# Kernel tuning notes

Measured on AMD Instinct MI355X. Metric: run time of the kernel, lower is better.

Reference implementation:

```python
import jax, jax.numpy as jnp
import numpy as np

B, T, D, H = 4, 2048, 1024, 16
HD = D // H
EPS = 1e-5


def gelu_tanh(x):
    c = jnp.sqrt(jnp.asarray(2.0 / jnp.pi, x.dtype))
    return 0.5 * x * (1.0 + jnp.tanh(c * (x + 0.044715 * x * x * x)))


def layernorm(x, gamma, beta):
    mean = jnp.mean(x, axis=-1, keepdims=True)
    var = jnp.var(x, axis=-1, keepdims=True)
    return gamma * (x - mean) / jnp.sqrt(var + EPS) + beta


def setup_inputs() -> dict:
    key = jax.random.key(0)
    ks = jax.random.split(key, 12)
    s = 0.02
    return {
        "x": jax.random.normal(ks[0], (B, T, D), jnp.float32),
        "Wq": jax.random.normal(ks[1], (D, D), jnp.float32) * s,
        "Wk": jax.random.normal(ks[2], (D, D), jnp.float32) * s,
        "Wv": jax.random.normal(ks[3], (D, D), jnp.float32) * s,
        "Wo": jax.random.normal(ks[4], (D, D), jnp.float32) * s,
        "bo": jnp.zeros((D,), jnp.float32),
        "W1": jax.random.normal(ks[5], (D, 4 * D), jnp.float32) * s,
        "b1": jnp.zeros((4 * D,), jnp.float32),
        "W2": jax.random.normal(ks[6], (4 * D, D), jnp.float32) * s,
        "b2": jnp.zeros((D,), jnp.float32),
        "gamma1": jnp.ones((D,), jnp.float32),
        "beta1": jnp.zeros((D,), jnp.float32),
        "gamma2": jnp.ones((D,), jnp.float32),
        "beta2": jnp.zeros((D,), jnp.float32),
    }


def reference(x, Wq, Wk, Wv, Wo, bo, W1, b1, W2, b2, gamma1, beta1, gamma2, beta2):
    # --- attention sublayer (pre-norm, causal) ---
    h = layernorm(x, gamma1, beta1)
    q = (h @ Wq).reshape(B, T, H, HD).transpose(0, 2, 1, 3)  # (B,H,T,hd)
    k = (h @ Wk).reshape(B, T, H, HD).transpose(0, 2, 1, 3)
    v = (h @ Wv).reshape(B, T, H, HD).transpose(0, 2, 1, 3)
    scores = jnp.einsum("bhqd,bhkd->bhqk", q, k) * (HD ** -0.5)
    causal = jnp.tril(jnp.ones((T, T), bool))
    scores = jnp.where(causal, scores, -jnp.inf)
    w = jax.nn.softmax(scores, axis=-1)
    attn = jnp.einsum("bhqk,bhkd->bhqd", w, v).transpose(0, 2, 1, 3).reshape(B, T, D)
    x = x + (attn @ Wo + bo)
    # --- FFN sublayer ---
    h2 = layernorm(x, gamma2, beta2)
    ff = gelu_tanh(h2 @ W1 + b1) @ W2 + b2
    return x + ff
```

## Files before the change

kernel.cpp:

```cpp
#include <hip/hip_runtime.h>
#include <hip/hip_bf16.h>


typedef __bf16 bf16;
typedef __attribute__((ext_vector_type(8))) __bf16 bf16x8;
typedef __attribute__((ext_vector_type(4))) __bf16 bf16x4;
typedef __attribute__((ext_vector_type(2))) __bf16 bf16x2;
typedef __attribute__((ext_vector_type(4))) float floatx4;

#define EXPC 0.18033688011112042f

__device__ __forceinline__ void async_cp16(const bf16* g, bf16* l) {
  __builtin_amdgcn_global_load_lds(
      (const __attribute__((address_space(1))) void*)g,
      (__attribute__((address_space(3))) void*)l, 16, 0, 0);
}

__global__ __launch_bounds__(256) void transpose_cvt4(
    const float* __restrict__ S0, const float* __restrict__ S1,
    const float* __restrict__ S2, const float* __restrict__ S3,
    bf16* __restrict__ D0, bf16* __restrict__ D1, bf16* __restrict__ D2,
    bf16* __restrict__ D3, int K, int N) {
  const float* W = (blockIdx.z == 0) ? S0 : (blockIdx.z == 1) ? S1
                   : (blockIdx.z == 2) ? S2 : S3;
  bf16* WT = (blockIdx.z == 0) ? D0 : (blockIdx.z == 1) ? D1
             : (blockIdx.z == 2) ? D2 : D3;
  __shared__ bf16 tile[32][33];
  const int tn = blockIdx.x;
  const int tk = blockIdx.y;
  const int t = threadIdx.x;
  const int row = t >> 3;
  const int c4 = (t & 7) * 4;

  const float* src = W + (size_t)(tk * 32 + row) * N + tn * 32 + c4;
  float4 v = *(const float4*)src;
  tile[row][c4 + 0] = (bf16)v.x;
  tile[row][c4 + 1] = (bf16)v.y;
  tile[row][c4 + 2] = (bf16)v.z;
  tile[row][c4 + 3] = (bf16)v.w;
  __syncthreads();
  bf16x4 o;
  o[0] = tile[c4 + 0][row];
  o[1] = tile[c4 + 1][row];
  o[2] = tile[c4 + 2][row];
  o[3] = tile[c4 + 3][row];
  *(bf16x4*)(WT + (size_t)(tn * 32 + row) * K + tk * 32 + c4) = o;
}

__global__ __launch_bounds__(256) void transpose_cvt(
    const float* __restrict__ W, bf16* __restrict__ WT, int K, int N) {
  __shared__ bf16 tile[32][33];
  const int tn = blockIdx.x;
  const int tk = blockIdx.y;
  const int t = threadIdx.x;
  const int row = t >> 3;
  const int c4 = (t & 7) * 4;

  const float* src = W + (size_t)(tk * 32 + row) * N + tn * 32 + c4;
  float4 v = *(const float4*)src;
  tile[row][c4 + 0] = (bf16)v.x;
  tile[row][c4 + 1] = (bf16)v.y;
  tile[row][c4 + 2] = (bf16)v.z;
  tile[row][c4 + 3] = (bf16)v.w;
  __syncthreads();
  bf16x4 o;
  o[0] = tile[c4 + 0][row];
  o[1] = tile[c4 + 1][row];
  o[2] = tile[c4 + 2][row];
  o[3] = tile[c4 + 3][row];
  *(bf16x4*)(WT + (size_t)(tn * 32 + row) * K + tk * 32 + c4) = o;
}

__global__ __launch_bounds__(256) void ln_kernel(
    const float* __restrict__ x, const float* __restrict__ gamma,
    const float* __restrict__ beta, bf16* __restrict__ out) {
  const int row = blockIdx.x;
  const int t = threadIdx.x;
  const float* xr = x + (size_t)row * 1024;
  float4 v4 = *(const float4*)(xr + t * 4);
  float a[4] = {v4.x, v4.y, v4.z, v4.w};
  float s = a[0] + a[1] + a[2] + a[3];
  float ss = a[0] * a[0] + a[1] * a[1] + a[2] * a[2] + a[3] * a[3];
  for (int off = 1; off < 64; off <<= 1) {
    s += __shfl_xor(s, off);
    ss += __shfl_xor(ss, off);
  }
  __shared__ float red[8];
  const int wid = t >> 6, lane = t & 63;
  if (lane == 0) { red[wid] = s; red[wid + 4] = ss; }
  __syncthreads();
  s = red[0] + red[1] + red[2] + red[3];
  ss = red[4] + red[5] + red[6] + red[7];
  const float mean = s * (1.0f / 1024.0f);
  const float var = ss * (1.0f / 1024.0f) - mean * mean;
  const float rstd = rsqrtf(var + 1e-5f);
  bf16x4 o;
  for (int j = 0; j < 4; ++j) {
    float g = gamma[t * 4 + j];
    float b = beta[t * 4 + j];
    o[j] = (bf16)((a[j] - mean) * rstd * g + b);
  }
  *(bf16x4*)(out + (size_t)row * 1024 + t * 4) = o;
}

__device__ __forceinline__ float gelu_f(float x) {
  const float c = 0.7978845608028654f;
  float u = c * (x + 0.044715f * x * x * x);
  u = fminf(fmaxf(u, -10.0f), 10.0f);
  float t = __builtin_exp2f(u * 2.8853900817779268f);
  return x * t * __builtin_amdgcn_rcpf(t + 1.0f);
}

template <int MODE, int BK>
__global__ __launch_bounds__(256, 2) void gemm_bt(
    const bf16* __restrict__ A, const bf16* __restrict__ BT,
    const float* __restrict__ bias, const float* __restrict__ resid,
    void* __restrict__ out, int M, int N, int K) {
  __shared__ bf16 sA[128 * BK];
  __shared__ bf16 sB[128 * BK];
  constexpr int GPR = BK / 8;
  constexpr int CPT = GPR / 2;
  constexpr int RPI = 256 / GPR;
  constexpr int SW = (BK >= 64) ? 7 : 0;

  const int t = threadIdx.x;
  const int lane = t & 63, wid = t >> 6;
  const int waveM = wid >> 1, waveN = wid & 1;
  const int quad = lane >> 4, l16 = lane & 15;
  const size_t m0 = (size_t)blockIdx.x * 128;
  const size_t n0 = (size_t)blockIdx.y * 128;

  floatx4 acc[4][4] = {};

  const int r0 = t / GPR;
  const int gp = t % GPR;
  const int gsrc = gp ^ (r0 & SW);
  const bf16* Ag = A + (m0 + r0) * (size_t)K + gsrc * 8;
  const bf16* Bg = BT + (n0 + r0) * (size_t)K + gsrc * 8;
  bf16* sAp = sA + t * 8;
  bf16* sBp = sB + t * 8;

  for (int k0 = 0; k0 < K; k0 += BK) {
    __syncthreads();
#pragma unroll
    for (int it = 0; it < CPT; ++it) {
      async_cp16(Ag + k0 + (size_t)(it * RPI) * K, sAp + it * 2048);
      async_cp16(Bg + k0 + (size_t)(it * RPI) * K, sBp + it * 2048);
    }
    __syncthreads();
#pragma unroll
    for (int ks = 0; ks < BK / 32; ++ks) {
      bf16x8 af[4], bfv[4];
#pragma unroll
      for (int i = 0; i < 4; ++i) {
        const int rowA = waveM * 64 + i * 16 + l16;
        const int g = ((ks * 4 + quad) ^ (l16 & SW)) * 8;
        af[i] = *(const bf16x8*)&sA[rowA * BK + g];
        const int rowB = waveN * 64 + i * 16 + l16;
        bfv[i] = *(const bf16x8*)&sB[rowB * BK + g];
      }
#pragma unroll
      for (int mt = 0; mt < 4; ++mt)
#pragma unroll
        for (int nt = 0; nt < 4; ++nt)
          acc[mt][nt] = __builtin_amdgcn_mfma_f32_16x16x32_bf16(
              af[mt], bfv[nt], acc[mt][nt], 0, 0, 0);
    }
  }

#pragma unroll
  for (int mt = 0; mt < 4; ++mt) {
#pragma unroll
    for (int nt = 0; nt < 4; ++nt) {
      const size_t row_base = m0 + waveM * 64 + mt * 16 + quad * 4;
      const size_t col = n0 + waveN * 64 + nt * 16 + l16;
#pragma unroll
      for (int r = 0; r < 4; ++r) {
        const size_t row = row_base + r;
        float v = acc[mt][nt][r];
        if (MODE == 1) {
          v = gelu_f(v + bias[col]);
          ((bf16*)out)[row * N + col] = (bf16)v;
        } else if (MODE == 2) {
          v += bias[col] + resid[row * N + col];
          ((float*)out)[row * N + col] = v;
        } else {
          ((bf16*)out)[row * N + col] = (bf16)v;
        }
      }
    }
  }
}

__global__ __launch_bounds__(256) void attn_kernel(
    const bf16* __restrict__ QKV, bf16* __restrict__ O) {
  const int idx = blockIdx.x;
  const int qt = 15 - (idx >> 6);
  const int bh = idx & 63;
  const int b = bh >> 4, h = bh & 15;
  const int t = threadIdx.x;
  const int lane = t & 63, wid = t >> 6;
  const int quad = lane >> 4, l16 = lane & 15;

  __shared__ bf16 sQ[128][72];
  __shared__ bf16 sK[64][72];
  __shared__ bf16 sVt[64][72];
  __shared__ bf16 sP[4][16][72];

  const size_t qbase = (size_t)b * 2048 * 3072 + (size_t)h * 64;
  const int q0 = qt * 128;

  for (int c = t; c < 1024; c += 256) {
    int row = c >> 3, sub = (c & 7) * 8;
    *(bf16x8*)&sQ[row][sub] =
        *(const bf16x8*)(QKV + qbase + (size_t)(q0 + row) * 3072 + sub);
  }
  __syncthreads();

  bf16x8 aq[2][2];
#pragma unroll
  for (int mt = 0; mt < 2; ++mt)
#pragma unroll
    for (int ks = 0; ks < 2; ++ks)
      aq[mt][ks] =
          *(const bf16x8*)&sQ[wid * 32 + mt * 16 + l16][ks * 32 + quad * 8];

  float l_part[2][4] = {};
  floatx4 o_acc[2][4] = {};

  const int kr = t >> 3;
  const int sub = (t & 7) * 8;
  const bf16* pK0 = QKV + qbase + 1024 + (size_t)kr * 3072 + sub;
  const bf16* pK1 = pK0 + (size_t)32 * 3072;
  const int vr = kr * 2;
  const bf16* pV0 = QKV + qbase + 2048 + (size_t)vr * 3072 + sub;
  const bf16* pV1 = pV0 + 3072;
  const int vcol = vr ^ (sub & 56);
  const ptrdiff_t bump = (ptrdiff_t)64 * 3072;

  const int ktmax = 2 * qt + 1;
  for (int kt = 0; kt <= ktmax; ++kt) {
    __syncthreads();
    *(bf16x8*)&sK[kr][sub] = *(const bf16x8*)pK0;
    *(bf16x8*)&sK[32 + kr][sub] = *(const bf16x8*)pK1;
    bf16x8 va = *(const bf16x8*)pV0;
    bf16x8 vb = *(const bf16x8*)pV1;
#pragma unroll
    for (int j = 0; j < 8; ++j) {
      bf16x2 pk = {va[j], vb[j]};
      *(bf16x2*)&sVt[sub + j][vcol] = pk;
    }
    pK0 += bump; pK1 += bump; pV0 += bump; pV1 += bump;
    __syncthreads();

    bf16x8 bv[4][2];
#pragma unroll
    for (int nt = 0; nt < 4; ++nt) {
      const int r2 = nt * 16 + l16;
#pragma unroll
      for (int ks = 0; ks < 2; ++ks)
        bv[nt][ks] =
            *(const bf16x8*)&sVt[r2][(ks * 32 + quad * 8) ^ (r2 & 56)];
    }

    float p[2][4][4];
#pragma unroll
    for (int nt = 0; nt < 4; ++nt) {
      const int r2 = nt * 16 + l16;
      bf16x8 bk0 = *(const bf16x8*)&sK[r2][quad * 8];
      bf16x8 bk1 = *(const bf16x8*)&sK[r2][32 + quad * 8];
#pragma unroll
      for (int mt = 0; mt < 2; ++mt) {
        floatx4 acc = {};
        acc = __builtin_amdgcn_mfma_f32_16x16x32_bf16(aq[mt][0], bk0, acc, 0, 0, 0);
        acc = __builtin_amdgcn_mfma_f32_16x16x32_bf16(aq[mt][1], bk1, acc, 0, 0, 0);
#pragma unroll
        for (int r = 0; r < 4; ++r)
          p[mt][nt][r] = __builtin_exp2f(acc[r] * EXPC);
      }
    }

    if (kt >= ktmax - 1) {
      const int k0 = kt * 64;
#pragma unroll
      for (int mt = 0; mt < 2; ++mt) {
        const int qrow_base = q0 + wid * 32 + mt * 16 + quad * 4;
#pragma unroll
        for (int nt = 0; nt < 4; ++nt) {
          const int kk = k0 + nt * 16 + l16;
#pragma unroll
          for (int r = 0; r < 4; ++r)
            if (kk > qrow_base + r) p[mt][nt][r] = 0.f;
        }
      }
    }

#pragma unroll
    for (int mt = 0; mt < 2; ++mt) {
#pragma unroll
      for (int nt = 0; nt < 4; ++nt)
#pragma unroll
        for (int r = 0; r < 4; ++r) {
          l_part[mt][r] += p[mt][nt][r];
          sP[wid][quad * 4 + r][nt * 16 + l16] = (bf16)p[mt][nt][r];
        }
      bf16x8 ap0 = *(const bf16x8*)&sP[wid][l16][quad * 8];
      bf16x8 ap1 = *(const bf16x8*)&sP[wid][l16][32 + quad * 8];
#pragma unroll
      for (int nt = 0; nt < 4; ++nt) {
        o_acc[mt][nt] = __builtin_amdgcn_mfma_f32_16x16x32_bf16(
            ap0, bv[nt][0], o_acc[mt][nt], 0, 0, 0);
        o_acc[mt][nt] = __builtin_amdgcn_mfma_f32_16x16x32_bf16(
            ap1, bv[nt][1], o_acc[mt][nt], 0, 0, 0);
      }
    }
  }

#pragma unroll
  for (int mt = 0; mt < 2; ++mt) {
#pragma unroll
    for (int off = 1; off < 16; off <<= 1)
#pragma unroll
      for (int r = 0; r < 4; ++r)
        l_part[mt][r] += __shfl_xor(l_part[mt][r], off);
    float inv[4];
#pragma unroll
    for (int r = 0; r < 4; ++r) inv[r] = 1.0f / l_part[mt][r];
#pragma unroll
    for (int nt = 0; nt < 4; ++nt)
#pragma unroll
      for (int r = 0; r < 4; ++r) {
        const size_t row =
            (size_t)b * 2048 + q0 + wid * 32 + mt * 16 + quad * 4 + r;
        const size_t col = (size_t)h * 64 + nt * 16 + l16;
        O[row * 1024 + col] = (bf16)(o_acc[mt][nt][r] * inv[r]);
      }
  }
}

extern "C" void kernel_launch(void* const* d_in, const int* in_sizes, int n_in,
                              void* d_out, int out_size, void* d_ws, size_t ws_size,
                              hipStream_t stream) {
  const float* x = (const float*)d_in[0];
  const float* Wq = (const float*)d_in[1];
  const float* Wk = (const float*)d_in[2];
  const float* Wv = (const float*)d_in[3];
  const float* Wo = (const float*)d_in[4];
  const float* bo = (const float*)d_in[5];
  const float* W1 = (const float*)d_in[6];
  const float* b1 = (const float*)d_in[7];
  const float* W2 = (const float*)d_in[8];
  const float* b2 = (const float*)d_in[9];
  const float* gamma1 = (const float*)d_in[10];
  const float* beta1 = (const float*)d_in[11];
  const float* gamma2 = (const float*)d_in[12];
  const float* beta2 = (const float*)d_in[13];

  char* ws = (char*)d_ws;
  const size_t MB = (size_t)1 << 20;
  bf16* WqkvT = (bf16*)(ws + 0 * MB);
  bf16* WoT = (bf16*)(ws + 6 * MB);
  bf16* W1T = (bf16*)(ws + 8 * MB);
  bf16* W2T = (bf16*)(ws + 16 * MB);
  bf16* h1  = (bf16*)(ws + 24 * MB);
  bf16* QKVb = (bf16*)(ws + 40 * MB);
  bf16* attnb = (bf16*)(ws + 88 * MB);
  float* x1 = (float*)(ws + 104 * MB);
  bf16* h2  = (bf16*)(ws + 136 * MB);
  bf16* midb = (bf16*)(ws + 152 * MB);

  dim3 blk(256);

  transpose_cvt4<<<dim3(32, 32, 4), blk, 0, stream>>>(
      Wq, Wk, Wv, Wo, WqkvT, WqkvT + (size_t)1024 * 1024,
      WqkvT + (size_t)2048 * 1024, WoT, 1024, 1024);
  transpose_cvt<<<dim3(128, 32), blk, 0, stream>>>(W1, W1T, 1024, 4096);
  transpose_cvt<<<dim3(32, 128), blk, 0, stream>>>(W2, W2T, 4096, 1024);

  ln_kernel<<<8192, blk, 0, stream>>>(x, gamma1, beta1, h1);

  gemm_bt<3, 64><<<dim3(64, 24), blk, 0, stream>>>(h1, WqkvT, nullptr, nullptr,
                                                   QKVb, 8192, 3072, 1024);

  attn_kernel<<<dim3(1024), blk, 0, stream>>>(QKVb, attnb);

  gemm_bt<2, 128><<<dim3(64, 8), blk, 0, stream>>>(attnb, WoT, bo, x, x1,
                                                   8192, 1024, 1024);

  ln_kernel<<<8192, blk, 0, stream>>>(x1, gamma2, beta2, h2);

  gemm_bt<1, 64><<<dim3(64, 32), blk, 0, stream>>>(h2, W1T, b1, nullptr, midb,
                                                   8192, 4096, 1024);

  gemm_bt<2, 128><<<dim3(64, 8), blk, 0, stream>>>(midb, W2T, b2, x1, d_out,
                                                   8192, 1024, 4096);
}
```

Measured before the change: 468.0 us.

## Pre-transpose V and use async global-to-LDS loads with XOR swizzle in attention

Adds a separate kernel that writes V transposed per head into workspace, which removes the in-loop scalar transpose-scatter into LDS. The attention kernel now loads Q, K and V^T straight into LDS with global_load_lds and an XOR-swizzled layout, and swaps the MFMA operands so P is stored as packed bf16x4 with a simpler row-sum reduction. The cost is an extra kernel launch and an extra pass over V through memory. Vt reuses h1's workspace region, which is already consumed by then.

```diff
diff --git a/kernel.cpp b/kernel.cpp
--- a/kernel.cpp
+++ b/kernel.cpp
@@ -5,7 +5,6 @@
 typedef __bf16 bf16;
 typedef __attribute__((ext_vector_type(8))) __bf16 bf16x8;
 typedef __attribute__((ext_vector_type(4))) __bf16 bf16x4;
-typedef __attribute__((ext_vector_type(2))) __bf16 bf16x2;
 typedef __attribute__((ext_vector_type(4))) float floatx4;
 
 #define EXPC 0.18033688011112042f
@@ -69,6 +68,31 @@
   o[2] = tile[c4 + 2][row];
   o[3] = tile[c4 + 3][row];
   *(bf16x4*)(WT + (size_t)(tn * 32 + row) * K + tk * 32 + c4) = o;
+}
+
+__global__ __launch_bounds__(256) void vtrans_kernel(
+    const bf16* __restrict__ QKV, bf16* __restrict__ Vt) {
+  const int tt = blockIdx.x;
+  const int bh = blockIdx.y;
+  const int b = bh >> 4, h = bh & 15;
+  __shared__ bf16 tile[64][72];
+  const int t = threadIdx.x;
+  const int row = t >> 3;
+  const int c8 = (t & 7) * 8;
+  const size_t vbase = (size_t)b * 2048 * 3072 + 2048 + (size_t)h * 64;
+  const bf16* src = QKV + vbase + (size_t)(tt * 64 + row) * 3072 + c8;
+  *(bf16x8*)&tile[row][c8] = *(const bf16x8*)src;
+  *(bf16x8*)&tile[row + 32][c8] = *(const bf16x8*)(src + (size_t)32 * 3072);
+  __syncthreads();
+  bf16x8 o0, o1;
+#pragma unroll
+  for (int j = 0; j < 8; ++j) {
+    o0[j] = tile[c8 + j][row];
+    o1[j] = tile[c8 + j][row + 32];
+  }
+  bf16* dst = Vt + ((size_t)bh * 64 + row) * 2048 + tt * 64 + c8;
+  *(bf16x8*)dst = o0;
+  *(bf16x8*)(dst + (size_t)32 * 2048) = o1;
 }
 
 __global__ __launch_bounds__(256) void ln_kernel(
@@ -193,7 +217,8 @@
 }
 
 __global__ __launch_bounds__(256) void attn_kernel(
-    const bf16* __restrict__ QKV, bf16* __restrict__ O) {
+    const bf16* __restrict__ QKV, const bf16* __restrict__ Vt,
+    bf16* __restrict__ O) {
   const int idx = blockIdx.x;
   const int qt = 15 - (idx >> 6);
   const int bh = idx & 63;
@@ -202,78 +227,76 @@
   const int lane = t & 63, wid = t >> 6;
   const int quad = lane >> 4, l16 = lane & 15;
 
-  __shared__ bf16 sQ[128][72];
-  __shared__ bf16 sK[64][72];
-  __shared__ bf16 sVt[64][72];
+  __shared__ bf16 sQ[128 * 64];
+  __shared__ bf16 sK[64 * 64];
+  __shared__ bf16 sV[64 * 64];
   __shared__ bf16 sP[4][16][72];
 
-  const size_t qbase = (size_t)b * 2048 * 3072 + (size_t)h * 64;
+  const size_t qkvbase = (size_t)b * 2048 * 3072 + (size_t)h * 64;
   const int q0 = qt * 128;
 
-  for (int c = t; c < 1024; c += 256) {
-    int row = c >> 3, sub = (c & 7) * 8;
-    *(bf16x8*)&sQ[row][sub] =
-        *(const bf16x8*)(QKV + qbase + (size_t)(q0 + row) * 3072 + sub);
-  }
+  const int r0 = t >> 3;
+  const int gp = t & 7;
+  const int gsw = gp ^ (r0 & 7);
+
+  {
+    const bf16* pQ = QKV + qkvbase + (size_t)(q0 + r0) * 3072 + gsw * 8;
+#pragma unroll
+    for (int j = 0; j < 4; ++j)
+      async_cp16(pQ + (size_t)(j * 32) * 3072, sQ + j * 2048 + t * 8);
+  }
+
+  const bf16* pK = QKV + qkvbase + 1024 + (size_t)r0 * 3072 + gsw * 8;
+  const bf16* pV = Vt + ((size_t)bh * 64 + r0) * 2048 + gsw * 8;
+  const ptrdiff_t bumpK = (ptrdiff_t)64 * 3072;
+
   __syncthreads();
 
   bf16x8 aq[2][2];
 #pragma unroll
-  for (int mt = 0; mt < 2; ++mt)
+  for (int mt = 0; mt < 2; ++mt) {
+    const int row = wid * 32 + mt * 16 + l16;
 #pragma unroll
     for (int ks = 0; ks < 2; ++ks)
       aq[mt][ks] =
-          *(const bf16x8*)&sQ[wid * 32 + mt * 16 + l16][ks * 32 + quad * 8];
-
-  float l_part[2][4] = {};
+          *(const bf16x8*)&sQ[row * 64 + (((ks * 4 + quad) ^ (row & 7)) * 8)];
+  }
+
+  float l_part[2] = {0.f, 0.f};
   floatx4 o_acc[2][4] = {};
-
-  const int kr = t >> 3;
-  const int sub = (t & 7) * 8;
-  const bf16* pK0 = QKV + qbase + 1024 + (size_t)kr * 3072 + sub;
-  const bf16* pK1 = pK0 + (size_t)32 * 3072;
-  const int vr = kr * 2;
-  const bf16* pV0 = QKV + qbase + 2048 + (size_t)vr * 3072 + sub;
-  const bf16* pV1 = pV0 + 3072;
-  const int vcol = vr ^ (sub & 56);
-  const ptrdiff_t bump = (ptrdiff_t)64 * 3072;
 
   const int ktmax = 2 * qt + 1;
   for (int kt = 0; kt <= ktmax; ++kt) {
     __syncthreads();
-    *(bf16x8*)&sK[kr][sub] = *(const bf16x8*)pK0;
-    *(bf16x8*)&sK[32 + kr][sub] = *(const bf16x8*)pK1;
-    bf16x8 va = *(const bf16x8*)pV0;
-    bf16x8 vb = *(const bf16x8*)pV1;
-#pragma unroll
-    for (int j = 0; j < 8; ++j) {
-      bf16x2 pk = {va[j], vb[j]};
-      *(bf16x2*)&sVt[sub + j][vcol] = pk;
-    }
-    pK0 += bump; pK1 += bump; pV0 += bump; pV1 += bump;
+    async_cp16(pK, sK + t * 8);
+    async_cp16(pK + (size_t)32 * 3072, sK + 2048 + t * 8);
+    async_cp16(pV, sV + t * 8);
+    async_cp16(pV + (size_t)32 * 2048, sV + 2048 + t * 8);
+    pK += bumpK;
+    pV += 64;
     __syncthreads();
 
     bf16x8 bv[4][2];
 #pragma unroll
     for (int nt = 0; nt < 4; ++nt) {
-      const int r2 = nt * 16 + l16;
+      const int d = nt * 16 + l16;
 #pragma unroll
       for (int ks = 0; ks < 2; ++ks)
         bv[nt][ks] =
-            *(const bf16x8*)&sVt[r2][(ks * 32 + quad * 8) ^ (r2 & 56)];
+            *(const bf16x8*)&sV[d * 64 + (((ks * 4 + quad) ^ (d & 7)) * 8)];
     }
 
     float p[2][4][4];
 #pragma unroll
     for (int nt = 0; nt < 4; ++nt) {
-      const int r2 = nt * 16 + l16;
-      bf16x8 bk0 = *(const bf16x8*)&sK[r2][quad * 8];
-      bf16x8 bk1 = *(const bf16x8*)&sK[r2][32 + quad * 8];
+      const int kr = nt * 16 + l16;
+      bf16x8 bk0 = *(const bf16x8*)&sK[kr * 64 + ((quad ^ (kr & 7)) * 8)];
+      bf16x8 bk1 = *(const bf16x8*)&sK[kr * 64 + (((4 + quad) ^ (kr & 7)) * 8)];
 #pragma unroll
       for (int mt = 0; mt < 2; ++mt) {
         floatx4 acc = {};
-        acc = __builtin_amdgcn_mfma_f32_16x16x32_bf16(aq[mt][0], bk0, acc, 0, 0, 0);
-        acc = __builtin_amdgcn_mfma_f32_16x16x32_bf16(aq[mt][1], bk1, acc, 0, 0, 0);
+        acc = __builtin_amdgcn_mfma_f32_16x16x32_bf16(bk0, aq[mt][0], acc, 0, 0, 0);
+        acc = __builtin_amdgcn_mfma_f32_16x16x32_bf16(bk1, aq[mt][1], acc, 0, 0, 0);
 #pragma unroll
         for (int r = 0; r < 4; ++r)
           p[mt][nt][r] = __builtin_exp2f(acc[r] * EXPC);
@@ -284,13 +307,13 @@
       const int k0 = kt * 64;
 #pragma unroll
       for (int mt = 0; mt < 2; ++mt) {
-        const int qrow_base = q0 + wid * 32 + mt * 16 + quad * 4;
+        const int qg = q0 + wid * 32 + mt * 16 + l16;
 #pragma unroll
         for (int nt = 0; nt < 4; ++nt) {
-          const int kk = k0 + nt * 16 + l16;
+          const int kg = k0 + nt * 16 + quad * 4;
 #pragma unroll
           for (int r = 0; r < 4; ++r)
-            if (kk > qrow_base + r) p[mt][nt][r] = 0.f;
+            if (kg + r > qg) p[mt][nt][r] = 0.f;
         }
       }
     }
@@ -298,12 +321,15 @@
 #pragma unroll
     for (int mt = 0; mt < 2; ++mt) {
 #pragma unroll
-      for (int nt = 0; nt < 4; ++nt)
+      for (int nt = 0; nt < 4; ++nt) {
+        bf16x4 pk;
 #pragma unroll
         for (int r = 0; r < 4; ++r) {
-          l_part[mt][r] += p[mt][nt][r];
-          sP[wid][quad * 4 + r][nt * 16 + l16] = (bf16)p[mt][nt][r];
+          l_part[mt] += p[mt][nt][r];
+          pk[r] = (bf16)p[mt][nt][r];
         }
+        *(bf16x4*)&sP[wid][l16][nt * 16 + quad * 4] = pk;
+      }
       bf16x8 ap0 = *(const bf16x8*)&sP[wid][l16][quad * 8];
       bf16x8 ap1 = *(const bf16x8*)&sP[wid][l16][32 + quad * 8];
 #pragma unroll
@@ -318,14 +344,13 @@
 
 #pragma unroll
   for (int mt = 0; mt < 2; ++mt) {
-#pragma unroll
-    for (int off = 1; off < 16; off <<= 1)
-#pragma unroll
-      for (int r = 0; r < 4; ++r)
-        l_part[mt][r] += __shfl_xor(l_part[mt][r], off);
+    float lt = l_part[mt];
+    lt += __shfl_xor(lt, 16);
+    lt += __shfl_xor(lt, 32);
     float inv[4];
 #pragma unroll
-    for (int r = 0; r < 4; ++r) inv[r] = 1.0f / l_part[mt][r];
+    for (int r = 0; r < 4; ++r)
+      inv[r] = 1.0f / __shfl(lt, quad * 4 + r);
 #pragma unroll
     for (int nt = 0; nt < 4; ++nt)
 #pragma unroll
@@ -363,6 +388,7 @@
   bf16* W1T = (bf16*)(ws + 8 * MB);
   bf16* W2T = (bf16*)(ws + 16 * MB);
   bf16* h1  = (bf16*)(ws + 24 * MB);
+  bf16* Vt  = (bf16*)(ws + 24 * MB);
   bf16* QKVb = (bf16*)(ws + 40 * MB);
   bf16* attnb = (bf16*)(ws + 88 * MB);
   float* x1 = (float*)(ws + 104 * MB);
@@ -382,7 +408,9 @@
   gemm_bt<3, 64><<<dim3(64, 24), blk, 0, stream>>>(h1, WqkvT, nullptr, nullptr,
                                                    QKVb, 8192, 3072, 1024);
 
-  attn_kernel<<<dim3(1024), blk, 0, stream>>>(QKVb, attnb);
+  vtrans_kernel<<<dim3(32, 64), blk, 0, stream>>>(QKVb, Vt);
+
+  attn_kernel<<<dim3(1024), blk, 0, stream>>>(QKVb, Vt, attnb);
 
   gemm_bt<2, 128><<<dim3(64, 8), blk, 0, stream>>>(attnb, WoT, bo, x, x1,
                                                    8192, 1024, 1024);
```

After: 452.8 us. -3.2%, faster.
